# Kernel tuning notes

Hardware: AMD Instinct MI355X
Metric: run time of the kernel (lower is better)

Reference implementation:

```python
import jax, jax.numpy as jnp
from jax import lax
import numpy as np

NUM_HEADS = 12


def setup_inputs() -> dict:
    key = jax.random.key(0)
    ks = jax.random.split(key, 7)
    B, H, W, C = 8, 32, 32, 384
    x = jax.random.normal(ks[0], (B, H, W, C), dtype=jnp.float32)
    cls_token = jax.random.normal(ks[1], (B, 1, C), dtype=jnp.float32)
    qkv_w = jax.random.normal(ks[2], (3 * C, C), dtype=jnp.float32) * 0.02
    proj_w = jax.random.normal(ks[3], (C, C), dtype=jnp.float32) * 0.02
    proj_b = jax.random.normal(ks[4], (C,), dtype=jnp.float32) * 0.02
    lepe_w = jax.random.normal(ks[5], (C, 1, 5, 5), dtype=jnp.float32) * 0.02
    lepe_b = jax.random.normal(ks[6], (C,), dtype=jnp.float32) * 0.02
    return {"x": x, "cls_token": cls_token, "qkv_w": qkv_w,
            "proj_w": proj_w, "proj_b": proj_b,
            "lepe_w": lepe_w, "lepe_b": lepe_b}


def reference(x, cls_token, qkv_w, proj_w, proj_b, lepe_w, lepe_b):
    B, H, W, C = x.shape
    nh = NUM_HEADS
    hd = C // nh
    scale = hd ** (-0.5)

    x_seq = x.reshape(B, H * W, C)                      # [B, N, C]
    x_cat = jnp.concatenate([cls_token, x_seq], axis=1)  # [B, N+1, C]
    N1 = x_cat.shape[1]

    qkv = (x_cat @ qkv_w.T).reshape(B, N1, 3, nh, hd)
    qkv = qkv.transpose(2, 0, 3, 1, 4)                  # [3, B, h, N+1, d]
    q, k, v = qkv[0], qkv[1], qkv[2]

    attn = jnp.einsum('bhqd,bhkd->bhqk', q, k) * scale  # [B, h, N+1, N+1]
    attn = jax.nn.softmax(attn, axis=-1)
    out = jnp.einsum('bhqk,bhkd->bhqd', attn, v)        # [B, h, N+1, d]
    out = out.transpose(0, 2, 1, 3).reshape(B, N1, C)
    cls_out, x_out = out[:, :1, :], out[:, 1:, :]

    # LePE: 5x5 depthwise conv over the spatial grid (NCHW, groups=C)
    lepe = lax.conv_general_dilated(
        x.transpose(0, 3, 1, 2), lepe_w,
        window_strides=(1, 1), padding='SAME',
        feature_group_count=C,
        dimension_numbers=('NCHW', 'OIHW', 'NCHW'))
    lepe = lepe + lepe_b[None, :, None, None]
    lepe = lepe.transpose(0, 2, 3, 1).reshape(B, H * W, C)

    x_out = (x_out + lepe) @ proj_w.T + proj_b
    cls_out = cls_out @ proj_w.T + proj_b
    return x_out.reshape(B, H, W, C), cls_out
```

## Files before the change

### kernel.cpp

```cpp
#include <hip/hip_runtime.h>
#include <math.h>

#define NB 8
#define NHH 32
#define NWW 32
#define NC 384
#define NHEAD 12
#define NHD 32
#define NN1 1025
#define NHW 1024
#define NMROWS (NB * NN1)
#define MPAD 8320
#define NPB 1088
#define MP2 (NB * NPB)
#define NMT (MP2 / 64)
#define CST 1152
#define NBH (NB * NHEAD)
#define QTILES 17

typedef float f32x4 __attribute__((ext_vector_type(4)));
typedef __bf16 bf16x8 __attribute__((ext_vector_type(8)));
typedef __bf16 bf16x4 __attribute__((ext_vector_type(4)));
typedef short s16x4 __attribute__((ext_vector_type(4)));
typedef __attribute__((address_space(3))) unsigned int lds_u32;
typedef const __attribute__((address_space(1))) unsigned int glb_u32;

static __device__ __forceinline__ bf16x8 as_bf16x8(uint4 u) {
    union { uint4 a; bf16x8 b; } x; x.a = u; return x.b;
}
static __device__ __forceinline__ unsigned short bfbits(__bf16 b) {
    union { __bf16 a; unsigned short s; } u; u.a = b; return u.s;
}
static __device__ __forceinline__ float bf2f(unsigned short s) {
    union { unsigned u; float f; } x; x.u = ((unsigned)s) << 16; return x.f;
}
static __device__ __forceinline__ unsigned pack2(float a, float b) {
    return (unsigned)bfbits((__bf16)a) | ((unsigned)bfbits((__bf16)b) << 16);
}
static __device__ __forceinline__ float fexp2(float x) {
    return __builtin_amdgcn_exp2f(x);
}
static __device__ __forceinline__ f32x4 mfma16(bf16x4 a, bf16x4 b, f32x4 c) {
#if __has_builtin(__builtin_amdgcn_mfma_f32_16x16x16_bf16)
    return __builtin_amdgcn_mfma_f32_16x16x16_bf16(a, b, c, 0, 0, 0);
#else
    union { bf16x4 h; s16x4 s; } ua, ub; ua.h = a; ub.h = b;
    return __builtin_amdgcn_mfma_f32_16x16x16bf16_1k(ua.s, ub.s, c, 0, 0, 0);
#endif
}
static __device__ __forceinline__ int xcd_swz(int i, int nwg) {
    int xcd = i & 7, pos = i >> 3;
    int q = nwg >> 3, r = nwg & 7;
    return xcd * q + (xcd < r ? xcd : r) + pos;
}

#define P_N1 835584
#define P_N2 110592
#define P_N3 36864
#define P_N4 9600
#define P_N5 11520
#define P_TOT (P_N1 + P_N2 + P_N3 + P_N4 + P_N5)

__global__ __launch_bounds__(256) void prep_k(
    const float* __restrict__ x, const float* __restrict__ cls,
    const float* __restrict__ qkv_w, const float* __restrict__ proj_w,
    const float* __restrict__ lepe_w,
    __bf16* __restrict__ Ab, __bf16* __restrict__ wqb, __bf16* __restrict__ wpb,
    float* __restrict__ lepeT, __bf16* __restrict__ aob)
{
    int idx = blockIdx.x * 256 + threadIdx.x;
    if (idx >= P_TOT) return;
    if (idx < P_N1) {
        int e0 = idx * 4;
        int mp = e0 / NC, kk = e0 % NC;
        int b = mp / NPB, n = mp % NPB;
        float4 v = make_float4(0.f, 0.f, 0.f, 0.f);
        if (n < NN1) {
            const float* src = (n == 0) ? (cls + (size_t)b * NC + kk)
                                        : (x + ((size_t)(b * NHW + (n - 1))) * NC + kk);
            v = *(const float4*)src;
        }
        uint2 u; u.x = pack2(v.x, v.y); u.y = pack2(v.z, v.w);
        *(uint2*)(Ab + (size_t)mp * NC + kk) = u;
        return;
    }
    idx -= P_N1;
    if (idx < P_N2) {
        int e0 = idx * 4;
        float4 v = *(const float4*)(qkv_w + e0);
        uint2 u; u.x = pack2(v.x, v.y); u.y = pack2(v.z, v.w);
        *(uint2*)(wqb + e0) = u;
        return;
    }
    idx -= P_N2;
    if (idx < P_N3) {
        int e0 = idx * 4;
        float4 v = *(const float4*)(proj_w + e0);
        uint2 u; u.x = pack2(v.x, v.y); u.y = pack2(v.z, v.w);
        *(uint2*)(wpb + e0) = u;
        return;
    }
    idx -= P_N3;
    if (idx < P_N4) {
        int tap = idx / NC, cc = idx % NC;
        lepeT[tap * NC + cc] = lepe_w[cc * 25 + tap];
        return;
    }
    idx -= P_N4;
    {
        uint2 z; z.x = 0; z.y = 0;
        *(uint2*)(aob + (size_t)NMROWS * NC + idx * 4) = z;
    }
}

#define LP 72
#define QSCALE 0.25505654007f
#define CPD 136

union QkvSm {
    struct { __bf16 As[2][64][64]; __bf16 Bs[2][128][64]; } g;
    __bf16 C[64][CPD];
};

__global__ __launch_bounds__(256) void qkv_mfma_k(
    const __bf16* __restrict__ A, const __bf16* __restrict__ W,
    __bf16* __restrict__ Cg)
{
    __shared__ QkvSm sm;
    const int tid  = threadIdx.x;
    const int lane = tid & 63;
    const int wid  = tid >> 6;
    const int wr   = wid >> 1, wc = wid & 1;
    const int c    = lane & 15, hg = lane >> 4;
    const int wg   = xcd_swz(blockIdx.x, 9 * NMT);
    const int tile = wg % 9;
    const int m0   = (wg / 9) * 64;
    const int n0   = tile * 128;

    int aw_row[2], aw_col[2];
#pragma unroll
    for (int j = 0; j < 2; ++j) {
        int word = (wid * 2 + j) * 64 + lane;
        int row = word >> 3, slot = word & 7;
        aw_row[j] = row;
        aw_col[j] = (slot ^ (row & 7)) * 8;
    }
    int bw_row[4], bw_col[4];
#pragma unroll
    for (int j = 0; j < 4; ++j) {
        int word = (wid * 4 + j) * 64 + lane;
        int row = word >> 3, slot = word & 7;
        bw_row[j] = row;
        bw_col[j] = (slot ^ (row & 7)) * 8;
    }

    f32x4 acc[2][4];
#pragma unroll
    for (int i = 0; i < 2; ++i)
#pragma unroll
        for (int j = 0; j < 4; ++j) acc[i][j] = f32x4{0.f, 0.f, 0.f, 0.f};

    __bf16* asbase = &sm.g.As[0][0][0];
    __bf16* bsbase = &sm.g.Bs[0][0][0];

    auto stage = [&](int buf, int k0) {
#pragma unroll
        for (int j = 0; j < 2; ++j) {
            const __bf16* src = A + (size_t)(m0 + aw_row[j]) * NC + k0 + aw_col[j];
            __bf16* dst = asbase + (size_t)buf * 4096 + (wid * 2 + j) * 512;
            __builtin_amdgcn_global_load_lds((glb_u32*)src, (lds_u32*)dst, 16, 0, 0);
        }
#pragma unroll
        for (int j = 0; j < 4; ++j) {
            const __bf16* src = W + (size_t)(n0 + bw_row[j]) * NC + k0 + bw_col[j];
            __bf16* dst = bsbase + (size_t)buf * 8192 + (wid * 4 + j) * 512;
            __builtin_amdgcn_global_load_lds((glb_u32*)src, (lds_u32*)dst, 16, 0, 0);
        }
    };

    stage(0, 0);
    __syncthreads();

    for (int t = 0; t < 6; ++t) {
        const int cur = t & 1;
        if (t < 5) stage(cur ^ 1, (t + 1) * 64);

        const __bf16* ab = asbase + (size_t)cur * 4096;
        const __bf16* bb = bsbase + (size_t)cur * 8192;
#pragma unroll
        for (int ks = 0; ks < 2; ++ks) {
            bf16x8 af[2], bfr[4];
#pragma unroll
            for (int i = 0; i < 2; ++i) {
                int row = wr * 32 + i * 16 + c;
                int slot = (ks * 4 + hg) ^ (row & 7);
                af[i] = as_bf16x8(*(const uint4*)(ab + row * 64 + slot * 8));
            }
#pragma unroll
            for (int j = 0; j < 4; ++j) {
                int row = wc * 64 + j * 16 + c;
                int slot = (ks * 4 + hg) ^ (row & 7);
                bfr[j] = as_bf16x8(*(const uint4*)(bb + row * 64 + slot * 8));
            }
            __builtin_amdgcn_s_setprio(1);
#pragma unroll
            for (int i = 0; i < 2; ++i)
#pragma unroll
                for (int j = 0; j < 4; ++j)
                    acc[i][j] = __builtin_amdgcn_mfma_f32_16x16x32_bf16(
                        af[i], bfr[j], acc[i][j], 0, 0, 0);
            __builtin_amdgcn_s_setprio(0);
        }
        if (t < 5) __syncthreads();
    }

    __syncthreads();
    const float qs = (tile < 3) ? QSCALE : 1.0f;
#pragma unroll
    for (int i = 0; i < 2; ++i)
#pragma unroll
        for (int r = 0; r < 4; ++r) {
            int row = wr * 32 + i * 16 + 4 * hg + r;
#pragma unroll
            for (int j = 0; j < 4; ++j)
                sm.C[row][wc * 64 + j * 16 + c] = (__bf16)(acc[i][j][r] * qs);
        }
    __syncthreads();

#pragma unroll
    for (int it = 0; it < 4; ++it) {
        int idx   = it * 256 + tid;
        int row   = idx >> 4;
        int chunk = idx & 15;
        uint4 u = *(const uint4*)&sm.C[row][chunk * 8];
        *(uint4*)(Cg + (size_t)(m0 + row) * CST + n0 + chunk * 8) = u;
    }
}

__global__ __launch_bounds__(256) void proj_mfma_k(
    const __bf16* __restrict__ A, const __bf16* __restrict__ W,
    const float* __restrict__ bias, float* __restrict__ out)
{
    __shared__ __bf16 As[128][LP];
    __shared__ __bf16 Bs[64][LP];
    const int tid  = threadIdx.x;
    const int lane = tid & 63;
    const int wid  = tid >> 6;
    const int wr   = wid >> 1, wc = wid & 1;
    const int c    = lane & 15, hg = lane >> 4;
    const int wg   = xcd_swz(blockIdx.x, 6 * 65);
    const int m0   = (wg / 6) * 128;
    const int n0   = (wg % 6) * 64;
    const int srow = tid >> 1;
    const int scol = (tid & 1) * 32;
    const int brow = tid >> 2;
    const int bcol = (tid & 3) * 16;

    f32x4 acc[4][2];
#pragma unroll
    for (int i = 0; i < 4; ++i)
#pragma unroll
        for (int j = 0; j < 2; ++j) acc[i][j] = f32x4{0.f, 0.f, 0.f, 0.f};

    uint4 a4[4], b4[2];
#pragma unroll
    for (int s = 0; s < 4; ++s)
        a4[s] = *(const uint4*)(A + (size_t)(m0 + srow) * NC + scol + s * 8);
#pragma unroll
    for (int s = 0; s < 2; ++s)
        b4[s] = *(const uint4*)(W + (size_t)(n0 + brow) * NC + bcol + s * 8);

    for (int k0 = 0; k0 < NC; k0 += 64) {
        __syncthreads();
#pragma unroll
        for (int s = 0; s < 4; ++s) *(uint4*)&As[srow][scol + s * 8] = a4[s];
#pragma unroll
        for (int s = 0; s < 2; ++s) *(uint4*)&Bs[brow][bcol + s * 8] = b4[s];
        __syncthreads();
        if (k0 + 64 < NC) {
#pragma unroll
            for (int s = 0; s < 4; ++s)
                a4[s] = *(const uint4*)(A + (size_t)(m0 + srow) * NC + k0 + 64 + scol + s * 8);
#pragma unroll
            for (int s = 0; s < 2; ++s)
                b4[s] = *(const uint4*)(W + (size_t)(n0 + brow) * NC + k0 + 64 + bcol + s * 8);
        }
#pragma unroll
        for (int ks = 0; ks < 2; ++ks) {
            bf16x8 af[4], bfr[2];
#pragma unroll
            for (int i = 0; i < 4; ++i)
                af[i] = as_bf16x8(*(const uint4*)&As[wr * 64 + i * 16 + c][ks * 32 + hg * 8]);
#pragma unroll
            for (int j = 0; j < 2; ++j)
                bfr[j] = as_bf16x8(*(const uint4*)&Bs[wc * 32 + j * 16 + c][ks * 32 + hg * 8]);
#pragma unroll
            for (int i = 0; i < 4; ++i)
#pragma unroll
                for (int j = 0; j < 2; ++j)
                    acc[i][j] = __builtin_amdgcn_mfma_f32_16x16x32_bf16(
                        af[i], bfr[j], acc[i][j], 0, 0, 0);
        }
    }

#pragma unroll
    for (int i = 0; i < 4; ++i)
#pragma unroll
        for (int r = 0; r < 4; ++r) {
            int m = m0 + wr * 64 + i * 16 + 4 * hg + r;
            if (m >= NMROWS) continue;
            int b = m / NN1, n = m % NN1;
            float* dstrow = (n == 0)
                ? (out + (size_t)NB * NHW * NC + (size_t)b * NC)
                : (out + ((size_t)(b * NHW) + (n - 1)) * NC);
#pragma unroll
            for (int j = 0; j < 2; ++j) {
                int col = n0 + wc * 32 + j * 16 + c;
                dstrow[col] = acc[i][j][r] + bias[col];
            }
        }
}

#define KC 64
#define VPAD 72
#define NCH ((NN1 + KC - 1) / KC)

__global__ __launch_bounds__(256) void attn_mfma_k(
    const __bf16* __restrict__ Cg, __bf16* __restrict__ ao)
{
    __shared__ unsigned short Vs[2][32][VPAD];

    const int wg    = xcd_swz(blockIdx.x, QTILES * NBH);
    const int qtile = wg % QTILES;
    const int bh    = wg / QTILES;
    const int b     = bh / NHEAD;
    const int hh    = bh % NHEAD;
    const int tid   = threadIdx.x;
    const int lane  = tid & 63;
    const int wv    = tid >> 6;
    const int c     = lane & 15;
    const int hg    = lane >> 4;
    const int q0    = qtile * 64 + wv * 16;
    const size_t MBp = (size_t)b * NPB;

    const __bf16* qb = Cg + hh * 32;
    const __bf16* kb = Cg + 384 + hh * 32;
    const __bf16* vb = Cg + 768 + hh * 32;

    uint4 zero4 = make_uint4(0, 0, 0, 0);
    bf16x8 qf;
    {
        int row = q0 + c;
        uint4 u = (row < NN1)
            ? *(const uint4*)(qb + (MBp + row) * CST + hg * 8) : zero4;
        qf = as_bf16x8(u);
    }

    f32x4 O[2];
#pragma unroll
    for (int dt = 0; dt < 2; ++dt) O[dt] = f32x4{0.f, 0.f, 0.f, 0.f};
    float lrun = 0.f;

    const int k_row = tid >> 2;
    const int k_col = (tid & 3) * 8;

    uint4 kcur[4], knxt[4];
#pragma unroll
    for (int kt = 0; kt < 4; ++kt)
        kcur[kt] = *(const uint4*)(kb + (MBp + kt * 16 + c) * CST + hg * 8);
    uint4 vr = *(const uint4*)(vb + (MBp + k_row) * CST + k_col);
    {
        union { uint4 u; unsigned short s[8]; } vu; vu.u = vr;
#pragma unroll
        for (int j = 0; j < 8; ++j) Vs[0][k_col + j][k_row] = vu.s[j];
    }
    __syncthreads();

    for (int t = 0; t < NCH; ++t) {
        const int kt0 = t * KC;
        const int cur = t & 1;
        const bool haveNext = (t + 1 < NCH);
        if (haveNext) {
#pragma unroll
            for (int kt = 0; kt < 4; ++kt)
                knxt[kt] = *(const uint4*)(kb + (MBp + kt0 + KC + kt * 16 + c) * CST + hg * 8);
            vr = *(const uint4*)(vb + (MBp + kt0 + KC + k_row) * CST + k_col);
        }
        const bool full = (kt0 + KC <= NN1);

        f32x4 Sf[4];
        __builtin_amdgcn_s_setprio(1);
#pragma unroll
        for (int kt = 0; kt < 4; ++kt)
            Sf[kt] = __builtin_amdgcn_mfma_f32_16x16x32_bf16(
                as_bf16x8(kcur[kt]), qf, f32x4{0.f, 0.f, 0.f, 0.f}, 0, 0, 0);
        __builtin_amdgcn_s_setprio(0);

        if (!full) {
#pragma unroll
            for (int kt = 0; kt < 4; ++kt)
#pragma unroll
                for (int r = 0; r < 4; ++r) {
                    int key = kt0 + kt * 16 + 4 * hg + r;
                    if (key >= NN1) Sf[kt][r] = -3.0e38f;
                }
        }
        bf16x4 pa[4];
        float psum = 0.f;
#pragma unroll
        for (int kt = 0; kt < 4; ++kt) {
            float p0 = fexp2(Sf[kt][0]);
            float p1 = fexp2(Sf[kt][1]);
            float p2 = fexp2(Sf[kt][2]);
            float p3 = fexp2(Sf[kt][3]);
            psum += (p0 + p1) + (p2 + p3);
            pa[kt] = bf16x4{(__bf16)p0, (__bf16)p1, (__bf16)p2, (__bf16)p3};
        }
        lrun += psum;

        bf16x4 vbf[2][4];
#pragma unroll
        for (int dt = 0; dt < 2; ++dt)
#pragma unroll
            for (int kt = 0; kt < 4; ++kt)
                vbf[dt][kt] = *(const bf16x4*)&Vs[cur][dt * 16 + c][kt * 16 + 4 * hg];

        __builtin_amdgcn_s_setprio(1);
#pragma unroll
        for (int dt = 0; dt < 2; ++dt)
#pragma unroll
            for (int kt = 0; kt < 4; ++kt)
                O[dt] = mfma16(pa[kt], vbf[dt][kt], O[dt]);
        __builtin_amdgcn_s_setprio(0);

        if (haveNext) {
            union { uint4 u; unsigned short s[8]; } vu; vu.u = vr;
#pragma unroll
            for (int j = 0; j < 8; ++j) Vs[cur ^ 1][k_col + j][k_row] = vu.s[j];
#pragma unroll
            for (int kt = 0; kt < 4; ++kt) kcur[kt] = knxt[kt];
            __syncthreads();
        }
    }

    {
        float Ls = lrun;
        Ls += __shfl_xor(Ls, 16);
        Ls += __shfl_xor(Ls, 32);
#pragma unroll
        for (int r = 0; r < 4; ++r) {
            float lr_ = __shfl(Ls, 4 * hg + r);
            int row = q0 + 4 * hg + r;
            float inv = (lr_ > 0.f) ? 1.0f / lr_ : 0.f;
            if (row < NN1) {
#pragma unroll
                for (int dt = 0; dt < 2; ++dt)
                    ao[((size_t)(b * NN1 + row)) * NC + hh * NHD + dt * 16 + c]
                        = (__bf16)(O[dt][r] * inv);
            }
        }
    }
}

__global__ __launch_bounds__(256) void lepe2_k(
    const float* __restrict__ x, const float* __restrict__ wT,
    const float* __restrict__ bias, __bf16* __restrict__ ao)
{
    int idx = blockIdx.x * 256 + threadIdx.x;
    if (idx >= NB * (NHH / 2) * NWW * (NC / 4)) return;
    int cg = idx % (NC / 4);
    int c4 = cg * 4;
    int pos = idx / (NC / 4);
    int ww = pos % NWW;
    int hp = (pos / NWW) % (NHH / 2);
    int b = pos / (NWW * (NHH / 2));
    int hh = hp * 2;

    float4 bv = *(const float4*)(bias + c4);
    float a0[2], a1[2], a2[2], a3[2];
    a0[0] = bv.x; a1[0] = bv.y; a2[0] = bv.z; a3[0] = bv.w;
    a0[1] = bv.x; a1[1] = bv.y; a2[1] = bv.z; a3[1] = bv.w;

#pragma unroll
    for (int i = 0; i < 6; ++i) {
        int y = hh + i - 2;
        bool yv = (unsigned)y < NHH;
#pragma unroll
        for (int j = 0; j < 5; ++j) {
            int xw = ww + j - 2;
            if (yv && (unsigned)xw < NWW) {
                float4 xv = *(const float4*)(x + (((size_t)b * NHH + y) * NWW + xw) * NC + c4);
                if (i < 5) {
                    float4 wv = *(const float4*)(wT + (i * 5 + j) * NC + c4);
                    a0[0] += xv.x * wv.x; a1[0] += xv.y * wv.y;
                    a2[0] += xv.z * wv.z; a3[0] += xv.w * wv.w;
                }
                if (i >= 1) {
                    float4 wv = *(const float4*)(wT + ((i - 1) * 5 + j) * NC + c4);
                    a0[1] += xv.x * wv.x; a1[1] += xv.y * wv.y;
                    a2[1] += xv.z * wv.z; a3[1] += xv.w * wv.w;
                }
            }
        }
    }

#pragma unroll
    for (int rr = 0; rr < 2; ++rr) {
        size_t m = (size_t)b * NN1 + 1 + (hh + rr) * NWW + ww;
        uint2* aop = (uint2*)(ao + m * NC + c4);
        uint2 old = *aop;
        float r0 = a0[rr] + bf2f((unsigned short)(old.x & 0xffff));
        float r1 = a1[rr] + bf2f((unsigned short)(old.x >> 16));
        float r2 = a2[rr] + bf2f((unsigned short)(old.y & 0xffff));
        float r3 = a3[rr] + bf2f((unsigned short)(old.y >> 16));
        uint2 nw; nw.x = pack2(r0, r1); nw.y = pack2(r2, r3);
        *aop = nw;
    }
}

extern "C" void kernel_launch(void* const* d_in, const int* in_sizes, int n_in,
                              void* d_out, int out_size, void* d_ws, size_t ws_size,
                              hipStream_t stream)
{
    const float* x      = (const float*)d_in[0];
    const float* cls    = (const float*)d_in[1];
    const float* qkv_w  = (const float*)d_in[2];
    const float* proj_w = (const float*)d_in[3];
    const float* proj_b = (const float*)d_in[4];
    const float* lepe_w = (const float*)d_in[5];
    const float* lepe_b = (const float*)d_in[6];
    float* out = (float*)d_out;
    char*  ws  = (char*)d_ws;

    size_t off = 0;
    __bf16* Ab    = (__bf16*)(ws + off); off += (size_t)MP2 * NC * 2;
    __bf16* wqb   = (__bf16*)(ws + off); off += (size_t)1152 * NC * 2;
    __bf16* wpb   = (__bf16*)(ws + off); off += (size_t)NC * NC * 2;
    float*  lepeT = (float*) (ws + off); off += (size_t)25 * NC * 4;
    __bf16* Cg    = (__bf16*)(ws + off); off += (size_t)MP2 * CST * 2;
    __bf16* aob   = (__bf16*)(ws + off); off += (size_t)MPAD * NC * 2;

    {
        prep_k<<<(P_TOT + 255) / 256, 256, 0, stream>>>(
            x, cls, qkv_w, proj_w, lepe_w, Ab, wqb, wpb, lepeT, aob);
    }
    {
        qkv_mfma_k<<<9 * NMT, 256, 0, stream>>>(Ab, wqb, Cg);
    }
    {
        attn_mfma_k<<<QTILES * NBH, 256, 0, stream>>>(Cg, aob);
    }
    {
        int total = NB * (NHW / 2) * (NC / 4);
        lepe2_k<<<(total + 255) / 256, 256, 0, stream>>>(x, lepeT, lepe_b, aob);
    }
    {
        proj_mfma_k<<<6 * 65, 256, 0, stream>>>(aob, wpb, proj_b, out);
    }
}
```

Baseline: 132.5 us.

## Enlarge QKV GEMM M-tile to 128 and attention block to 128 queries

The QKV GEMM now computes 128x128 output tiles per workgroup, with each wave holding a 4x4 accumulator grid. This raises reuse of the weight tiles and halves the grid. The attention kernel moves to 512-thread blocks covering 128 queries, staging two 64-key V chunks per barrier. This shares K/V loads across twice as many queries and halves the number of __syncthreads. The costs are more register pressure, fewer workgroups (864 attention blocks, 612 GEMM blocks), and a ragged last query tile where part of the block does wasted work.

```diff
diff --git a/kernel.cpp b/kernel.cpp
--- a/kernel.cpp
+++ b/kernel.cpp
@@ -13,10 +13,9 @@
 #define MPAD 8320
 #define NPB 1088
 #define MP2 (NB * NPB)
-#define NMT (MP2 / 64)
+#define NMT2 (MP2 / 128)
 #define CST 1152
 #define NBH (NB * NHEAD)
-#define QTILES 17
 
 typedef float f32x4 __attribute__((ext_vector_type(4)));
 typedef __bf16 bf16x8 __attribute__((ext_vector_type(8)));
@@ -115,11 +114,11 @@
 
 #define LP 72
 #define QSCALE 0.25505654007f
-#define CPD 136
+#define CPD2 132
 
 union QkvSm {
-    struct { __bf16 As[2][64][64]; __bf16 Bs[2][128][64]; } g;
-    __bf16 C[64][CPD];
+    struct { __bf16 As[2][128][64]; __bf16 Bs[2][128][64]; } g;
+    __bf16 C[128][CPD2];
 };
 
 __global__ __launch_bounds__(256) void qkv_mfma_k(
@@ -132,31 +131,23 @@
     const int wid  = tid >> 6;
     const int wr   = wid >> 1, wc = wid & 1;
     const int c    = lane & 15, hg = lane >> 4;
-    const int wg   = xcd_swz(blockIdx.x, 9 * NMT);
+    const int wg   = xcd_swz(blockIdx.x, 9 * NMT2);
     const int tile = wg % 9;
-    const int m0   = (wg / 9) * 64;
+    const int m0   = (wg / 9) * 128;
     const int n0   = tile * 128;
 
-    int aw_row[2], aw_col[2];
-#pragma unroll
-    for (int j = 0; j < 2; ++j) {
-        int word = (wid * 2 + j) * 64 + lane;
-        int row = word >> 3, slot = word & 7;
-        aw_row[j] = row;
-        aw_col[j] = (slot ^ (row & 7)) * 8;
-    }
-    int bw_row[4], bw_col[4];
+    int sw_row[4], sw_col[4];
 #pragma unroll
     for (int j = 0; j < 4; ++j) {
         int word = (wid * 4 + j) * 64 + lane;
         int row = word >> 3, slot = word & 7;
-        bw_row[j] = row;
-        bw_col[j] = (slot ^ (row & 7)) * 8;
-    }
-
-    f32x4 acc[2][4];
-#pragma unroll
-    for (int i = 0; i < 2; ++i)
+        sw_row[j] = row;
+        sw_col[j] = (slot ^ (row & 7)) * 8;
+    }
+
+    f32x4 acc[4][4];
+#pragma unroll
+    for (int i = 0; i < 4; ++i)
 #pragma unroll
         for (int j = 0; j < 4; ++j) acc[i][j] = f32x4{0.f, 0.f, 0.f, 0.f};
 
@@ -165,16 +156,13 @@
 
     auto stage = [&](int buf, int k0) {
 #pragma unroll
-        for (int j = 0; j < 2; ++j) {
-            const __bf16* src = A + (size_t)(m0 + aw_row[j]) * NC + k0 + aw_col[j];
-            __bf16* dst = asbase + (size_t)buf * 4096 + (wid * 2 + j) * 512;
-            __builtin_amdgcn_global_load_lds((glb_u32*)src, (lds_u32*)dst, 16, 0, 0);
-        }
-#pragma unroll
         for (int j = 0; j < 4; ++j) {
-            const __bf16* src = W + (size_t)(n0 + bw_row[j]) * NC + k0 + bw_col[j];
-            __bf16* dst = bsbase + (size_t)buf * 8192 + (wid * 4 + j) * 512;
-            __builtin_amdgcn_global_load_lds((glb_u32*)src, (lds_u32*)dst, 16, 0, 0);
+            const __bf16* srcA = A + (size_t)(m0 + sw_row[j]) * NC + k0 + sw_col[j];
+            __bf16* dstA = asbase + (size_t)buf * 8192 + (wid * 4 + j) * 512;
+            __builtin_amdgcn_global_load_lds((glb_u32*)srcA, (lds_u32*)dstA, 16, 0, 0);
+            const __bf16* srcB = W + (size_t)(n0 + sw_row[j]) * NC + k0 + sw_col[j];
+            __bf16* dstB = bsbase + (size_t)buf * 8192 + (wid * 4 + j) * 512;
+            __builtin_amdgcn_global_load_lds((glb_u32*)srcB, (lds_u32*)dstB, 16, 0, 0);
         }
     };
 
@@ -185,14 +173,14 @@
         const int cur = t & 1;
         if (t < 5) stage(cur ^ 1, (t + 1) * 64);
 
-        const __bf16* ab = asbase + (size_t)cur * 4096;
+        const __bf16* ab = asbase + (size_t)cur * 8192;
         const __bf16* bb = bsbase + (size_t)cur * 8192;
 #pragma unroll
         for (int ks = 0; ks < 2; ++ks) {
-            bf16x8 af[2], bfr[4];
-#pragma unroll
-            for (int i = 0; i < 2; ++i) {
-                int row = wr * 32 + i * 16 + c;
+            bf16x8 af[4], bfr[4];
+#pragma unroll
+            for (int i = 0; i < 4; ++i) {
+                int row = wr * 64 + i * 16 + c;
                 int slot = (ks * 4 + hg) ^ (row & 7);
                 af[i] = as_bf16x8(*(const uint4*)(ab + row * 64 + slot * 8));
             }
@@ -204,7 +192,7 @@
             }
             __builtin_amdgcn_s_setprio(1);
 #pragma unroll
-            for (int i = 0; i < 2; ++i)
+            for (int i = 0; i < 4; ++i)
 #pragma unroll
                 for (int j = 0; j < 4; ++j)
                     acc[i][j] = __builtin_amdgcn_mfma_f32_16x16x32_bf16(
@@ -217,10 +205,10 @@
     __syncthreads();
     const float qs = (tile < 3) ? QSCALE : 1.0f;
 #pragma unroll
-    for (int i = 0; i < 2; ++i)
+    for (int i = 0; i < 4; ++i)
 #pragma unroll
         for (int r = 0; r < 4; ++r) {
-            int row = wr * 32 + i * 16 + 4 * hg + r;
+            int row = wr * 64 + i * 16 + 4 * hg + r;
 #pragma unroll
             for (int j = 0; j < 4; ++j)
                 sm.C[row][wc * 64 + j * 16 + c] = (__bf16)(acc[i][j][r] * qs);
@@ -228,7 +216,7 @@
     __syncthreads();
 
 #pragma unroll
-    for (int it = 0; it < 4; ++it) {
+    for (int it = 0; it < 8; ++it) {
         int idx   = it * 256 + tid;
         int row   = idx >> 4;
         int chunk = idx & 15;
@@ -322,17 +310,17 @@
 }
 
 #define KC 64
-#define VPAD 72
-#define NCH ((NN1 + KC - 1) / KC)
-
-__global__ __launch_bounds__(256) void attn_mfma_k(
+#define VPAD 68
+#define NCH 17
+
+__global__ __launch_bounds__(512) void attn_mfma_k(
     const __bf16* __restrict__ Cg, __bf16* __restrict__ ao)
 {
-    __shared__ unsigned short Vs[2][32][VPAD];
-
-    const int wg    = xcd_swz(blockIdx.x, QTILES * NBH);
-    const int qtile = wg % QTILES;
-    const int bh    = wg / QTILES;
+    __shared__ unsigned short Vs[2][2][32][VPAD];
+
+    const int wg    = xcd_swz(blockIdx.x, 9 * NBH);
+    const int qtile = wg % 9;
+    const int bh    = wg / 9;
     const int b     = bh / NHEAD;
     const int hh    = bh % NHEAD;
     const int tid   = threadIdx.x;
@@ -340,7 +328,7 @@
     const int wv    = tid >> 6;
     const int c     = lane & 15;
     const int hg    = lane >> 4;
-    const int q0    = qtile * 64 + wv * 16;
+    const int q0    = qtile * 128 + wv * 16;
     const size_t MBp = (size_t)b * NPB;
 
     const __bf16* qb = Cg + hh * 32;
@@ -361,84 +349,100 @@
     for (int dt = 0; dt < 2; ++dt) O[dt] = f32x4{0.f, 0.f, 0.f, 0.f};
     float lrun = 0.f;
 
-    const int k_row = tid >> 2;
-    const int k_col = (tid & 3) * 8;
+    const int sub_s = tid >> 8;
+    const int t256  = tid & 255;
+    const int v_row = t256 >> 2;
+    const int v_col = (t256 & 3) * 8;
 
     uint4 kcur[4], knxt[4];
 #pragma unroll
     for (int kt = 0; kt < 4; ++kt)
         kcur[kt] = *(const uint4*)(kb + (MBp + kt * 16 + c) * CST + hg * 8);
-    uint4 vr = *(const uint4*)(vb + (MBp + k_row) * CST + k_col);
+    uint4 vr = *(const uint4*)(vb + (MBp + sub_s * KC + v_row) * CST + v_col);
     {
         union { uint4 u; unsigned short s[8]; } vu; vu.u = vr;
 #pragma unroll
-        for (int j = 0; j < 8; ++j) Vs[0][k_col + j][k_row] = vu.s[j];
+        for (int j = 0; j < 8; ++j) Vs[0][sub_s][v_col + j][v_row] = vu.s[j];
     }
     __syncthreads();
 
-    for (int t = 0; t < NCH; ++t) {
-        const int kt0 = t * KC;
-        const int cur = t & 1;
-        const bool haveNext = (t + 1 < NCH);
-        if (haveNext) {
+    for (int to = 0; to < 9; ++to) {
+        const int cur = to & 1;
+        const bool havePair = (to < 8);
+        if (havePair) {
+            int tn = 2 * to + 2 + sub_s;
+            vr = (tn < NCH)
+                ? *(const uint4*)(vb + (MBp + tn * KC + v_row) * CST + v_col)
+                : zero4;
+        }
+
+        for (int sub = 0; sub < 2; ++sub) {
+            const int t = 2 * to + sub;
+            if (t >= NCH) break;
+            const int kt0 = t * KC;
+            const bool haveK = (t + 1 < NCH);
+            if (haveK) {
+#pragma unroll
+                for (int kt = 0; kt < 4; ++kt)
+                    knxt[kt] = *(const uint4*)(kb + (MBp + kt0 + KC + kt * 16 + c) * CST + hg * 8);
+            }
+            const bool full = (kt0 + KC <= NN1);
+
+            f32x4 Sf[4];
+            __builtin_amdgcn_s_setprio(1);
 #pragma unroll
             for (int kt = 0; kt < 4; ++kt)
-                knxt[kt] = *(const uint4*)(kb + (MBp + kt0 + KC + kt * 16 + c) * CST + hg * 8);
-            vr = *(const uint4*)(vb + (MBp + kt0 + KC + k_row) * CST + k_col);
-        }
-        const bool full = (kt0 + KC <= NN1);
-
-        f32x4 Sf[4];
-        __builtin_amdgcn_s_setprio(1);
-#pragma unroll
-        for (int kt = 0; kt < 4; ++kt)
-            Sf[kt] = __builtin_amdgcn_mfma_f32_16x16x32_bf16(
-                as_bf16x8(kcur[kt]), qf, f32x4{0.f, 0.f, 0.f, 0.f}, 0, 0, 0);
-        __builtin_amdgcn_s_setprio(0);
-
-        if (!full) {
-#pragma unroll
-            for (int kt = 0; kt < 4; ++kt)
-#pragma unroll
-                for (int r = 0; r < 4; ++r) {
-                    int key = kt0 + kt * 16 + 4 * hg + r;
-                    if (key >= NN1) Sf[kt][r] = -3.0e38f;
-                }
-        }
-        bf16x4 pa[4];
-        float psum = 0.f;
-#pragma unroll
-        for (int kt = 0; kt < 4; ++kt) {
-            float p0 = fexp2(Sf[kt][0]);
-            float p1 = fexp2(Sf[kt][1]);
-            float p2 = fexp2(Sf[kt][2]);
-            float p3 = fexp2(Sf[kt][3]);
-            psum += (p0 + p1) + (p2 + p3);
-            pa[kt] = bf16x4{(__bf16)p0, (__bf16)p1, (__bf16)p2, (__bf16)p3};
-        }
-        lrun += psum;
-
-        bf16x4 vbf[2][4];
-#pragma unroll
-        for (int dt = 0; dt < 2; ++dt)
-#pragma unroll
-            for (int kt = 0; kt < 4; ++kt)
-                vbf[dt][kt] = *(const bf16x4*)&Vs[cur][dt * 16 + c][kt * 16 + 4 * hg];
-
-        __builtin_amdgcn_s_setprio(1);
-#pragma unroll
-        for (int dt = 0; dt < 2; ++dt)
-#pragma unroll
-            for (int kt = 0; kt < 4; ++kt)
-                O[dt] = mfma16(pa[kt], vbf[dt][kt], O[dt]);
-        __builtin_amdgcn_s_setprio(0);
-
-        if (haveNext) {
+                Sf[kt] = __builtin_amdgcn_mfma_f32_16x16x32_bf16(
+                    as_bf16x8(kcur[kt]), qf, f32x4{0.f, 0.f, 0.f, 0.f}, 0, 0, 0);
+            __builtin_amdgcn_s_setprio(0);
+
+            if (!full) {
+#pragma unroll
+                for (int kt = 0; kt < 4; ++kt)
+#pragma unroll
+                    for (int r = 0; r < 4; ++r) {
+                        int key = kt0 + kt * 16 + 4 * hg + r;
+                        if (key >= NN1) Sf[kt][r] = -3.0e38f;
+                    }
+            }
+            bf16x4 pa[4];
+            float psum = 0.f;
+#pragma unroll
+            for (int kt = 0; kt < 4; ++kt) {
+                float p0 = fexp2(Sf[kt][0]);
+                float p1 = fexp2(Sf[kt][1]);
+                float p2 = fexp2(Sf[kt][2]);
+                float p3 = fexp2(Sf[kt][3]);
+                psum += (p0 + p1) + (p2 + p3);
+                pa[kt] = bf16x4{(__bf16)p0, (__bf16)p1, (__bf16)p2, (__bf16)p3};
+            }
+            lrun += psum;
+
+            bf16x4 vbf[2][4];
+#pragma unroll
+            for (int dt = 0; dt < 2; ++dt)
+#pragma unroll
+                for (int kt = 0; kt < 4; ++kt)
+                    vbf[dt][kt] = *(const bf16x4*)&Vs[cur][sub][dt * 16 + c][kt * 16 + 4 * hg];
+
+            __builtin_amdgcn_s_setprio(1);
+#pragma unroll
+            for (int dt = 0; dt < 2; ++dt)
+#pragma unroll
+                for (int kt = 0; kt < 4; ++kt)
+                    O[dt] = mfma16(pa[kt], vbf[dt][kt], O[dt]);
+            __builtin_amdgcn_s_setprio(0);
+
+            if (haveK) {
+#pragma unroll
+                for (int kt = 0; kt < 4; ++kt) kcur[kt] = knxt[kt];
+            }
+        }
+
+        if (havePair) {
             union { uint4 u; unsigned short s[8]; } vu; vu.u = vr;
 #pragma unroll
-            for (int j = 0; j < 8; ++j) Vs[cur ^ 1][k_col + j][k_row] = vu.s[j];
-#pragma unroll
-            for (int kt = 0; kt < 4; ++kt) kcur[kt] = knxt[kt];
+            for (int j = 0; j < 8; ++j) Vs[cur ^ 1][sub_s][v_col + j][v_row] = vu.s[j];
             __syncthreads();
         }
     }
@@ -545,10 +549,10 @@
             x, cls, qkv_w, proj_w, lepe_w, Ab, wqb, wpb, lepeT, aob);
     }
     {
-        qkv_mfma_k<<<9 * NMT, 256, 0, stream>>>(Ab, wqb, Cg);
-    }
-    {
-        attn_mfma_k<<<QTILES * NBH, 256, 0, stream>>>(Cg, aob);
+        qkv_mfma_k<<<9 * NMT2, 256, 0, stream>>>(Ab, wqb, Cg);
+    }
+    {
+        attn_mfma_k<<<9 * NBH, 512, 0, stream>>>(Cg, aob);
     }
     {
         int total = NB * (NHW / 2) * (NC / 4);
```

Result: slower. 145.3 us (+9.6%).
